# Performance work log

Measured on AMD Instinct MI355X. Metric: run time of the kernel, lower is better.

Reference implementation:

```python
import jax, jax.numpy as jnp
import numpy as np

V, E, U, L = 50000, 512, 20, 9   # vocab, embed dim, user feats, labels
R, S, T = 64, 32, 50             # reviews, sentences/review, tokens/sentence
D = E + U                        # product-encoder input dim


def setup_inputs() -> dict:
    key = jax.random.key(0)
    ks = jax.random.split(key, 16)
    sc = lambda k, shape: (jax.random.normal(k, shape, jnp.float32) * 0.02)
    return {
        "inputs": jax.random.randint(ks[0], (R, S, T), 0, V),
        "user_feats": jax.random.normal(ks[1], (R, U), jnp.float32),
        "embedding": sc(ks[2], (V, E)),
        "w_sent": sc(ks[3], (E, E)), "b_sent": jnp.zeros((E,), jnp.float32),
        "w_rev": sc(ks[4], (E, E)),  "b_rev": jnp.zeros((E,), jnp.float32),
        "w_prod": sc(ks[5], (D, D)), "b_prod": jnp.zeros((D,), jnp.float32),
        "w_rff": sc(ks[6], (D, 1)),  "b_rff": jnp.zeros((1,), jnp.float32),
        "w_pff": sc(ks[7], (D, L)),  "b_pff": jnp.zeros((L,), jnp.float32),
        "user_w": jnp.ones((U,), jnp.float32),
    }


def _masked_mean(x, mask):
    # x: [..., N, F], mask: [..., N] -> [..., F]
    denom = jnp.maximum(mask.sum(-1, keepdims=True), 1.0)
    return (x * mask[..., None]).sum(-2) / denom


def reference(inputs, user_feats, embedding, w_sent, b_sent, w_rev, b_rev,
              w_prod, b_prod, w_rff, b_rff, w_pff, b_pff, user_w):
    dt = embedding.dtype
    tok_mask = (inputs != 0).astype(dt)                      # [R,S,T]
    emb = embedding[inputs]                                  # [R,S,T,E]
    # sentence encoder (DAN): masked mean over tokens + Linear + SELU
    sent_h = jax.nn.selu(_masked_mean(emb, tok_mask) @ w_sent + b_sent)   # [R,S,E]
    # review encoder: masked mean over sentences (r_mask = p.sum(-1) != 0)
    sent_mask = (inputs.sum(-1) != 0).astype(dt)             # [R,S]
    rev_h = jax.nn.selu(_masked_mean(sent_h, sent_mask) @ w_rev + b_rev)  # [R,E]
    # append L2-normalized user feats scaled by learned weights
    norm = jnp.sqrt((user_feats * user_feats).sum(-1, keepdims=True))
    uf = user_feats / jnp.maximum(norm, 1e-12) * user_w      # [R,U]
    p_batch = jnp.concatenate([rev_h, uf], axis=-1)          # [R,D]
    # per-review star head
    r_stars = jax.nn.selu(p_batch @ w_rff + b_rff).squeeze(-1)            # [R]
    # product encoder: plain mean over reviews (no mask) + Linear + SELU
    h_n = jax.nn.selu(p_batch.mean(-2) @ w_prod + b_prod)    # [D]
    p_stars = jax.nn.selu(h_n @ w_pff + b_pff)               # [L]
    return p_stars, r_stars
```

## Files before the change

kernel.cpp:

```cpp
#include <hip/hip_runtime.h>
#include <hip/hip_bf16.h>

#define R_ 64
#define S_ 32
#define T_ 50
#define E_ 512
#define U_ 20
#define D_ 532
#define L_ 9
#define NSENT (R_ * S_)

#define PCHUNK 128
#define NCG 5
#define NKG 5

typedef __attribute__((ext_vector_type(8))) short bf16x8;
typedef __attribute__((ext_vector_type(4))) float f32x4;

__device__ __forceinline__ float selu_f(float x) {
    const float scale = 1.0507009873554805f;
    const float alpha = 1.6732632423543772f;
    return x > 0.0f ? scale * x : scale * alpha * expm1f(x);
}

__global__ __launch_bounds__(256) void k_fused_A(
        const int* __restrict__ inputs,
        const float* __restrict__ emb,
        const float* __restrict__ w_sent,
        const float* __restrict__ w_rev,
        __hip_bfloat16* __restrict__ sent_bf,
        __hip_bfloat16* __restrict__ wT,
        float* __restrict__ smask,
        int* __restrict__ dcount)
{
    const int tid = threadIdx.x;

    if (blockIdx.x >= NSENT) {
        __shared__ float tile[32][33];
        const int b = blockIdx.x - NSENT;
        const int z = b >> 8;
        const float* w = z ? w_rev : w_sent;
        __hip_bfloat16* o = wT + (size_t)z * E_ * E_;
        const int bb = b & 255;
        const int tx = tid & 31, ty = tid >> 5;
        const int k0 = (bb >> 4) * 32, n0 = (bb & 15) * 32;
        #pragma unroll
        for (int i = 0; i < 4; ++i)
            tile[ty + 8 * i][tx] = w[(size_t)(k0 + ty + 8 * i) * E_ + n0 + tx];
        __syncthreads();
        #pragma unroll
        for (int i = 0; i < 4; ++i)
            o[(size_t)(n0 + ty + 8 * i) * E_ + k0 + tx] = __float2bfloat16(tile[tx][ty + 8 * i]);
        return;
    }

    if (blockIdx.x == 0 && tid == 0) *dcount = 0;

    const int sid = blockIdx.x;
    const int base = sid * T_;
    float2 acc = {0.f, 0.f};
    int cnt = 0;
    for (int t = 0; t < T_; ++t) {
        const int tok = inputs[base + t];
        const float m = (tok != 0) ? 1.0f : 0.0f;
        cnt += (tok != 0);
        const float2 v = ((const float2*)(emb + (size_t)tok * E_))[tid];
        acc.x = fmaf(v.x, m, acc.x);
        acc.y = fmaf(v.y, m, acc.y);
    }
    const float inv = 1.0f / fmaxf((float)cnt, 1.0f);
    __hip_bfloat162 h2;
    h2.x = __float2bfloat16(acc.x * inv);
    h2.y = __float2bfloat16(acc.y * inv);
    ((__hip_bfloat162*)(sent_bf + (size_t)sid * E_))[tid] = h2;
    if (tid == 0) smask[sid] = (cnt > 0) ? 1.0f : 0.0f;
}

__global__ __launch_bounds__(256) void k_gemm_sent_mean(
        const __hip_bfloat16* __restrict__ A,
        const __hip_bfloat16* __restrict__ Bt,
        const float* __restrict__ bias,
        const float* __restrict__ smask,
        __hip_bfloat16* __restrict__ mrev)
{
    __shared__ short As[64][40];
    __shared__ short Bs[64][40];
    const int tid  = threadIdx.x;
    const int wid  = tid >> 6;
    const int lane = tid & 63;
    const int wm = wid >> 1, wn = wid & 1;
    const int bm = blockIdx.y * 64, bn = blockIdx.x * 64;

    const int srow = tid >> 2;
    const int soff = (tid & 3) * 8;

    const short* Ag  = (const short*)A;
    const short* Btg = (const short*)Bt;

    f32x4 acc[2][2];
    #pragma unroll
    for (int i = 0; i < 2; ++i)
        #pragma unroll
        for (int j = 0; j < 2; ++j) acc[i][j] = (f32x4){0.f, 0.f, 0.f, 0.f};

    const int fr = lane & 15;
    const int kg = (lane >> 4) * 8;

    for (int k0 = 0; k0 < E_; k0 += 32) {
        __syncthreads();
        *(bf16x8*)&As[srow][soff] = *(const bf16x8*)&Ag[(size_t)(bm + srow) * E_ + k0 + soff];
        *(bf16x8*)&Bs[srow][soff] = *(const bf16x8*)&Btg[(size_t)(bn + srow) * E_ + k0 + soff];
        __syncthreads();
        bf16x8 af0 = *(const bf16x8*)&As[wm * 32 + fr][kg];
        bf16x8 af1 = *(const bf16x8*)&As[wm * 32 + 16 + fr][kg];
        bf16x8 bf0 = *(const bf16x8*)&Bs[wn * 32 + fr][kg];
        bf16x8 bf1 = *(const bf16x8*)&Bs[wn * 32 + 16 + fr][kg];
        acc[0][0] = __builtin_amdgcn_mfma_f32_16x16x32_bf16(af0, bf0, acc[0][0], 0, 0, 0);
        acc[0][1] = __builtin_amdgcn_mfma_f32_16x16x32_bf16(af0, bf1, acc[0][1], 0, 0, 0);
        acc[1][0] = __builtin_amdgcn_mfma_f32_16x16x32_bf16(af1, bf0, acc[1][0], 0, 0, 0);
        acc[1][1] = __builtin_amdgcn_mfma_f32_16x16x32_bf16(af1, bf1, acc[1][1], 0, 0, 0);
    }

    const int rq = (lane >> 4) * 4;
    float m[2][4];
    float msum = 0.f;
    #pragma unroll
    for (int fm = 0; fm < 2; ++fm)
        #pragma unroll
        for (int j = 0; j < 4; ++j) {
            m[fm][j] = smask[bm + wm * 32 + fm * 16 + rq + j];
            msum += m[fm][j];
        }
    float colsum[2];
    #pragma unroll
    for (int fn = 0; fn < 2; ++fn) {
        const float bv = bias[bn + wn * 32 + fn * 16 + fr];
        float s = 0.f;
        #pragma unroll
        for (int fm = 0; fm < 2; ++fm)
            #pragma unroll
            for (int j = 0; j < 4; ++j)
                s = fmaf(selu_f(acc[fm][fn][j] + bv), m[fm][j], s);
        colsum[fn] = s;
    }
    #pragma unroll
    for (int fn = 0; fn < 2; ++fn) {
        colsum[fn] += __shfl_xor(colsum[fn], 16, 64);
        colsum[fn] += __shfl_xor(colsum[fn], 32, 64);
    }
    msum += __shfl_xor(msum, 16, 64);
    msum += __shfl_xor(msum, 32, 64);
    const float inv = 1.0f / fmaxf(msum, 1.0f);
    if (lane < 16) {
        const int g = 2 * blockIdx.y + wm;
        #pragma unroll
        for (int fn = 0; fn < 2; ++fn)
            mrev[(size_t)g * E_ + bn + wn * 32 + fn * 16 + fr] =
                __float2bfloat16(colsum[fn] * inv);
    }
}

__global__ __launch_bounds__(256) void k_gemm_rev(
        const __hip_bfloat16* __restrict__ A,
        const __hip_bfloat16* __restrict__ Bt,
        const float* __restrict__ bias,
        const float* __restrict__ user_feats,
        const float* __restrict__ user_w,
        float* __restrict__ p_batch)
{
    __shared__ short As[64][40];
    __shared__ short Bs[64][40];
    const int tid  = threadIdx.x;
    const int wid  = tid >> 6;
    const int lane = tid & 63;
    const int wm = wid >> 1, wn = wid & 1;
    const int bn = blockIdx.x * 64;

    if (blockIdx.x == 0 && tid < 64) {
        const int r = tid;
        float ss = 0.f;
        #pragma unroll
        for (int j = 0; j < U_; ++j) {
            const float u = user_feats[r * U_ + j];
            ss = fmaf(u, u, ss);
        }
        const float nrm = fmaxf(sqrtf(ss), 1e-12f);
        #pragma unroll
        for (int j = 0; j < U_; ++j)
            p_batch[(size_t)r * D_ + E_ + j] = user_feats[r * U_ + j] / nrm * user_w[j];
    }

    const int srow = tid >> 2;
    const int soff = (tid & 3) * 8;
    const short* Ag  = (const short*)A;
    const short* Btg = (const short*)Bt;

    f32x4 acc[2][2];
    #pragma unroll
    for (int i = 0; i < 2; ++i)
        #pragma unroll
        for (int j = 0; j < 2; ++j) acc[i][j] = (f32x4){0.f, 0.f, 0.f, 0.f};

    const int fr = lane & 15;
    const int kg = (lane >> 4) * 8;

    for (int k0 = 0; k0 < E_; k0 += 32) {
        __syncthreads();
        *(bf16x8*)&As[srow][soff] = *(const bf16x8*)&Ag[(size_t)srow * E_ + k0 + soff];
        *(bf16x8*)&Bs[srow][soff] = *(const bf16x8*)&Btg[(size_t)(bn + srow) * E_ + k0 + soff];
        __syncthreads();
        bf16x8 af0 = *(const bf16x8*)&As[wm * 32 + fr][kg];
        bf16x8 af1 = *(const bf16x8*)&As[wm * 32 + 16 + fr][kg];
        bf16x8 bf0 = *(const bf16x8*)&Bs[wn * 32 + fr][kg];
        bf16x8 bf1 = *(const bf16x8*)&Bs[wn * 32 + 16 + fr][kg];
        acc[0][0] = __builtin_amdgcn_mfma_f32_16x16x32_bf16(af0, bf0, acc[0][0], 0, 0, 0);
        acc[0][1] = __builtin_amdgcn_mfma_f32_16x16x32_bf16(af0, bf1, acc[0][1], 0, 0, 0);
        acc[1][0] = __builtin_amdgcn_mfma_f32_16x16x32_bf16(af1, bf0, acc[1][0], 0, 0, 0);
        acc[1][1] = __builtin_amdgcn_mfma_f32_16x16x32_bf16(af1, bf1, acc[1][1], 0, 0, 0);
    }

    const int rq = (lane >> 4) * 4;
    #pragma unroll
    for (int fm = 0; fm < 2; ++fm) {
        #pragma unroll
        for (int fn = 0; fn < 2; ++fn) {
            const int col = bn + wn * 32 + fn * 16 + fr;
            const float bv = bias[col];
            #pragma unroll
            for (int j = 0; j < 4; ++j) {
                const int row = wm * 32 + fm * 16 + rq + j;
                p_batch[(size_t)row * D_ + col] = selu_f(acc[fm][fn][j] + bv);
            }
        }
    }
}

__global__ __launch_bounds__(256) void k_prod_fused(
        const float* __restrict__ p_batch,
        const float* __restrict__ w_prod,
        const float* __restrict__ b_prod,
        const float* __restrict__ w_pff,
        const float* __restrict__ b_pff,
        const float* __restrict__ w_rff,
        const float* __restrict__ b_rff,
        float* __restrict__ part,
        int* __restrict__ dcount,
        float* __restrict__ out_p,
        float* __restrict__ out_r)
{
    __shared__ float pbar[PCHUNK];
    __shared__ float red[2][PCHUNK];
    const int cg = blockIdx.x, kg = blockIdx.y;
    const int tid = threadIdx.x;
    const int cl = tid & (PCHUNK - 1);
    const int h  = tid >> 7;
    const int k0 = kg * PCHUNK;
    const int klen = min(PCHUNK, D_ - k0);

    if (cl < klen) {
        float s = 0.f;
        #pragma unroll 8
        for (int r = h * 32; r < h * 32 + 32; ++r)
            s += p_batch[(size_t)r * D_ + k0 + cl];
        red[h][cl] = s;
    }
    __syncthreads();
    if (h == 0 && cl < klen) pbar[cl] = (red[0][cl] + red[1][cl]) * (1.0f / 64.0f);
    __syncthreads();

    const int c = cg * PCHUNK + cl;
    float acc = 0.f;
    if (c < D_) {
        const int jb = h * 64;
        const int je = min(jb + 64, klen);
        for (int j = jb; j < je; ++j)
            acc = fmaf(pbar[j], w_prod[(size_t)(k0 + j) * D_ + c], acc);
    }
    red[h][cl] = acc;
    __syncthreads();
    if (h == 0 && c < D_) part[kg * D_ + c] = red[0][cl] + red[1][cl];

    __threadfence();
    __shared__ int is_last;
    if (tid == 0) is_last = (atomicAdd(dcount, 1) == NCG * NKG - 1);
    __syncthreads();
    if (!is_last) return;
    __threadfence();

    __shared__ float hn[D_];
    __shared__ float rred[4][64];
    for (int cc = tid; cc < D_; cc += 256) {
        float s = b_prod[cc];
        #pragma unroll
        for (int g = 0; g < NKG; ++g) s += part[g * D_ + cc];
        hn[cc] = selu_f(s);
    }
    __syncthreads();
    if (tid < L_) {
        float a = 0.f;
        for (int k = 0; k < D_; ++k) a = fmaf(hn[k], w_pff[k * L_ + tid], a);
        out_p[tid] = selu_f(a + b_pff[tid]);
    }
    {
        const int r = tid & 63, q = tid >> 6;
        float pr = 0.f;
        for (int k = q * 133; k < (q + 1) * 133; ++k)
            pr = fmaf(p_batch[(size_t)r * D_ + k], w_rff[k], pr);
        rred[q][r] = pr;
    }
    __syncthreads();
    if (tid < 64)
        out_r[tid] = selu_f(rred[0][tid] + rred[1][tid] + rred[2][tid] + rred[3][tid]
                            + b_rff[0]);
}

extern "C" void kernel_launch(void* const* d_in, const int* in_sizes, int n_in,
                              void* d_out, int out_size, void* d_ws, size_t ws_size,
                              hipStream_t stream) {
    const int*   inputs     = (const int*)  d_in[0];
    const float* user_feats = (const float*)d_in[1];
    const float* emb        = (const float*)d_in[2];
    const float* w_sent     = (const float*)d_in[3];
    const float* b_sent     = (const float*)d_in[4];
    const float* w_rev      = (const float*)d_in[5];
    const float* b_rev      = (const float*)d_in[6];
    const float* w_prod     = (const float*)d_in[7];
    const float* b_prod     = (const float*)d_in[8];
    const float* w_rff      = (const float*)d_in[9];
    const float* b_rff      = (const float*)d_in[10];
    const float* w_pff      = (const float*)d_in[11];
    const float* b_pff      = (const float*)d_in[12];
    const float* user_w     = (const float*)d_in[13];
    float* out = (float*)d_out;

    float* ws = (float*)d_ws;
    __hip_bfloat16* sent_bf = (__hip_bfloat16*)(ws);
    __hip_bfloat16* wT      = (__hip_bfloat16*)(ws + 524288);
    __hip_bfloat16* mrev    = (__hip_bfloat16*)(ws + 786432);
    float* smask   = ws + 802816;
    float* p_batch = ws + 804864;
    float* part    = ws + 838912;
    int*   dcount  = (int*)(ws + 841600);

    k_fused_A<<<NSENT + 512, 256, 0, stream>>>(inputs, emb, w_sent, w_rev,
                                               sent_bf, wT, smask, dcount);
    k_gemm_sent_mean<<<dim3(E_ / 64, NSENT / 64), 256, 0, stream>>>(
        sent_bf, wT, b_sent, smask, mrev);
    k_gemm_rev<<<dim3(E_ / 64, 1), 256, 0, stream>>>(
        mrev, wT + (size_t)E_ * E_, b_rev, user_feats, user_w, p_batch);
    k_prod_fused<<<dim3(NCG, NKG), 256, 0, stream>>>(
        p_batch, w_prod, b_prod, w_pff, b_pff, w_rff, b_rff,
        part, dcount, out, out + L_);
}
```

Before: 81.31 us.

## Fuse review-mean into rev GEMM epilogue and parallelize pff head

The review GEMM now computes the column means of p_batch (including the normalized user features) in its epilogue and writes them to a workspace vector. The product kernel loads that vector instead of re-reading and reducing p_batch in every block. The rev GEMM also uses a 64-wide K step, which halves its barrier count, and the final 9-output pff projection is split over 252 threads with a shared-memory reduction instead of running serially on 9 threads. This trims redundant work and serial tails in small latency-bound kernels, at the cost of extra shared memory and one more barrier in the GEMM.

```diff
diff --git a/kernel.cpp b/kernel.cpp
--- a/kernel.cpp
+++ b/kernel.cpp
@@ -90,21 +90,19 @@
     const int lane = tid & 63;
     const int wm = wid >> 1, wn = wid & 1;
     const int bm = blockIdx.y * 64, bn = blockIdx.x * 64;
-
     const int srow = tid >> 2;
     const int soff = (tid & 3) * 8;
-
     const short* Ag  = (const short*)A;
     const short* Btg = (const short*)Bt;
-
-    f32x4 acc[2][2];
-    #pragma unroll
-    for (int i = 0; i < 2; ++i)
-        #pragma unroll
-        for (int j = 0; j < 2; ++j) acc[i][j] = (f32x4){0.f, 0.f, 0.f, 0.f};
-
     const int fr = lane & 15;
     const int kg = (lane >> 4) * 8;
+    const int rq = (lane >> 4) * 4;
+
+    f32x4 acc[2][2];
+    #pragma unroll
+    for (int i = 0; i < 2; ++i)
+        #pragma unroll
+        for (int j = 0; j < 2; ++j) acc[i][j] = (f32x4){0.f, 0.f, 0.f, 0.f};
 
     for (int k0 = 0; k0 < E_; k0 += 32) {
         __syncthreads();
@@ -121,7 +119,6 @@
         acc[1][1] = __builtin_amdgcn_mfma_f32_16x16x32_bf16(af1, bf1, acc[1][1], 0, 0, 0);
     }
 
-    const int rq = (lane >> 4) * 4;
     float m[2][4];
     float msum = 0.f;
     #pragma unroll
@@ -166,15 +163,23 @@
         const float* __restrict__ bias,
         const float* __restrict__ user_feats,
         const float* __restrict__ user_w,
-        float* __restrict__ p_batch)
+        float* __restrict__ p_batch,
+        float* __restrict__ pbar)
 {
-    __shared__ short As[64][40];
-    __shared__ short Bs[64][40];
+    __shared__ short As[64][72];
+    __shared__ short Bs[64][72];
+    __shared__ float cs[2][2][2][16];
+    __shared__ float ufl[64][U_];
     const int tid  = threadIdx.x;
     const int wid  = tid >> 6;
     const int lane = tid & 63;
     const int wm = wid >> 1, wn = wid & 1;
     const int bn = blockIdx.x * 64;
+    const int fr = lane & 15;
+    const int kg = (lane >> 4) * 8;
+    const int rq = (lane >> 4) * 4;
+    const int srow = tid >> 2;
+    const int scol = (tid & 3) * 8;
 
     if (blockIdx.x == 0 && tid < 64) {
         const int r = tid;
@@ -186,12 +191,13 @@
         }
         const float nrm = fmaxf(sqrtf(ss), 1e-12f);
         #pragma unroll
-        for (int j = 0; j < U_; ++j)
-            p_batch[(size_t)r * D_ + E_ + j] = user_feats[r * U_ + j] / nrm * user_w[j];
-    }
-
-    const int srow = tid >> 2;
-    const int soff = (tid & 3) * 8;
+        for (int j = 0; j < U_; ++j) {
+            const float v = user_feats[r * U_ + j] / nrm * user_w[j];
+            p_batch[(size_t)r * D_ + E_ + j] = v;
+            ufl[r][j] = v;
+        }
+    }
+
     const short* Ag  = (const short*)A;
     const short* Btg = (const short*)Bt;
 
@@ -201,25 +207,27 @@
         #pragma unroll
         for (int j = 0; j < 2; ++j) acc[i][j] = (f32x4){0.f, 0.f, 0.f, 0.f};
 
-    const int fr = lane & 15;
-    const int kg = (lane >> 4) * 8;
-
-    for (int k0 = 0; k0 < E_; k0 += 32) {
-        __syncthreads();
-        *(bf16x8*)&As[srow][soff] = *(const bf16x8*)&Ag[(size_t)srow * E_ + k0 + soff];
-        *(bf16x8*)&Bs[srow][soff] = *(const bf16x8*)&Btg[(size_t)(bn + srow) * E_ + k0 + soff];
-        __syncthreads();
-        bf16x8 af0 = *(const bf16x8*)&As[wm * 32 + fr][kg];
-        bf16x8 af1 = *(const bf16x8*)&As[wm * 32 + 16 + fr][kg];
-        bf16x8 bf0 = *(const bf16x8*)&Bs[wn * 32 + fr][kg];
-        bf16x8 bf1 = *(const bf16x8*)&Bs[wn * 32 + 16 + fr][kg];
-        acc[0][0] = __builtin_amdgcn_mfma_f32_16x16x32_bf16(af0, bf0, acc[0][0], 0, 0, 0);
-        acc[0][1] = __builtin_amdgcn_mfma_f32_16x16x32_bf16(af0, bf1, acc[0][1], 0, 0, 0);
-        acc[1][0] = __builtin_amdgcn_mfma_f32_16x16x32_bf16(af1, bf0, acc[1][0], 0, 0, 0);
-        acc[1][1] = __builtin_amdgcn_mfma_f32_16x16x32_bf16(af1, bf1, acc[1][1], 0, 0, 0);
-    }
-
-    const int rq = (lane >> 4) * 4;
+    for (int k0 = 0; k0 < E_; k0 += 64) {
+        __syncthreads();
+        *(bf16x8*)&As[srow][scol]      = *(const bf16x8*)&Ag[(size_t)srow * E_ + k0 + scol];
+        *(bf16x8*)&As[srow][scol + 32] = *(const bf16x8*)&Ag[(size_t)srow * E_ + k0 + scol + 32];
+        *(bf16x8*)&Bs[srow][scol]      = *(const bf16x8*)&Btg[(size_t)(bn + srow) * E_ + k0 + scol];
+        *(bf16x8*)&Bs[srow][scol + 32] = *(const bf16x8*)&Btg[(size_t)(bn + srow) * E_ + k0 + scol + 32];
+        __syncthreads();
+        #pragma unroll
+        for (int ks = 0; ks < 64; ks += 32) {
+            bf16x8 af0 = *(const bf16x8*)&As[wm * 32 + fr][ks + kg];
+            bf16x8 af1 = *(const bf16x8*)&As[wm * 32 + 16 + fr][ks + kg];
+            bf16x8 bf0 = *(const bf16x8*)&Bs[wn * 32 + fr][ks + kg];
+            bf16x8 bf1 = *(const bf16x8*)&Bs[wn * 32 + 16 + fr][ks + kg];
+            acc[0][0] = __builtin_amdgcn_mfma_f32_16x16x32_bf16(af0, bf0, acc[0][0], 0, 0, 0);
+            acc[0][1] = __builtin_amdgcn_mfma_f32_16x16x32_bf16(af0, bf1, acc[0][1], 0, 0, 0);
+            acc[1][0] = __builtin_amdgcn_mfma_f32_16x16x32_bf16(af1, bf0, acc[1][0], 0, 0, 0);
+            acc[1][1] = __builtin_amdgcn_mfma_f32_16x16x32_bf16(af1, bf1, acc[1][1], 0, 0, 0);
+        }
+    }
+
+    float colsum[2] = {0.f, 0.f};
     #pragma unroll
     for (int fm = 0; fm < 2; ++fm) {
         #pragma unroll
@@ -229,13 +237,37 @@
             #pragma unroll
             for (int j = 0; j < 4; ++j) {
                 const int row = wm * 32 + fm * 16 + rq + j;
-                p_batch[(size_t)row * D_ + col] = selu_f(acc[fm][fn][j] + bv);
+                const float val = selu_f(acc[fm][fn][j] + bv);
+                p_batch[(size_t)row * D_ + col] = val;
+                colsum[fn] += val;
             }
         }
     }
+    #pragma unroll
+    for (int fn = 0; fn < 2; ++fn) {
+        colsum[fn] += __shfl_xor(colsum[fn], 16, 64);
+        colsum[fn] += __shfl_xor(colsum[fn], 32, 64);
+    }
+    if (lane < 16) {
+        cs[wm][wn][0][fr] = colsum[0];
+        cs[wm][wn][1][fr] = colsum[1];
+    }
+    __syncthreads();
+    if (tid < 64) {
+        const int wn2 = tid >> 5, fn2 = (tid >> 4) & 1, fr2 = tid & 15;
+        const float s = cs[0][wn2][fn2][fr2] + cs[1][wn2][fn2][fr2];
+        pbar[bn + wn2 * 32 + fn2 * 16 + fr2] = s * (1.0f / 64.0f);
+    }
+    if (blockIdx.x == 0 && tid < U_) {
+        float s = 0.f;
+        #pragma unroll 16
+        for (int r = 0; r < 64; ++r) s += ufl[r][tid];
+        pbar[E_ + tid] = s * (1.0f / 64.0f);
+    }
 }
 
 __global__ __launch_bounds__(256) void k_prod_fused(
+        const float* __restrict__ pbar_g,
         const float* __restrict__ p_batch,
         const float* __restrict__ w_prod,
         const float* __restrict__ b_prod,
@@ -248,7 +280,7 @@
         float* __restrict__ out_p,
         float* __restrict__ out_r)
 {
-    __shared__ float pbar[PCHUNK];
+    __shared__ float pb[PCHUNK];
     __shared__ float red[2][PCHUNK];
     const int cg = blockIdx.x, kg = blockIdx.y;
     const int tid = threadIdx.x;
@@ -257,15 +289,7 @@
     const int k0 = kg * PCHUNK;
     const int klen = min(PCHUNK, D_ - k0);
 
-    if (cl < klen) {
-        float s = 0.f;
-        #pragma unroll 8
-        for (int r = h * 32; r < h * 32 + 32; ++r)
-            s += p_batch[(size_t)r * D_ + k0 + cl];
-        red[h][cl] = s;
-    }
-    __syncthreads();
-    if (h == 0 && cl < klen) pbar[cl] = (red[0][cl] + red[1][cl]) * (1.0f / 64.0f);
+    if (tid < klen) pb[tid] = pbar_g[k0 + tid];
     __syncthreads();
 
     const int c = cg * PCHUNK + cl;
@@ -274,7 +298,7 @@
         const int jb = h * 64;
         const int je = min(jb + 64, klen);
         for (int j = jb; j < je; ++j)
-            acc = fmaf(pbar[j], w_prod[(size_t)(k0 + j) * D_ + c], acc);
+            acc = fmaf(pb[j], w_prod[(size_t)(k0 + j) * D_ + c], acc);
     }
     red[h][cl] = acc;
     __syncthreads();
@@ -289,6 +313,7 @@
 
     __shared__ float hn[D_];
     __shared__ float rred[4][64];
+    __shared__ float ppart[L_][28];
     for (int cc = tid; cc < D_; cc += 256) {
         float s = b_prod[cc];
         #pragma unroll
@@ -296,10 +321,12 @@
         hn[cc] = selu_f(s);
     }
     __syncthreads();
-    if (tid < L_) {
-        float a = 0.f;
-        for (int k = 0; k < D_; ++k) a = fmaf(hn[k], w_pff[k * L_ + tid], a);
-        out_p[tid] = selu_f(a + b_pff[tid]);
+    if (tid < L_ * 28) {
+        const int o = tid / 28, ii = tid % 28;
+        float s = 0.f;
+        for (int k = ii; k < D_; k += 28)
+            s = fmaf(hn[k], w_pff[(size_t)k * L_ + o], s);
+        ppart[o][ii] = s;
     }
     {
         const int r = tid & 63, q = tid >> 6;
@@ -309,6 +336,12 @@
         rred[q][r] = pr;
     }
     __syncthreads();
+    if (tid < L_) {
+        float s = 0.f;
+        #pragma unroll
+        for (int ii = 0; ii < 28; ++ii) s += ppart[tid][ii];
+        out_p[tid] = selu_f(s + b_pff[tid]);
+    }
     if (tid < 64)
         out_r[tid] = selu_f(rred[0][tid] + rred[1][tid] + rred[2][tid] + rred[3][tid]
                             + b_rff[0]);
@@ -340,15 +373,16 @@
     float* smask   = ws + 802816;
     float* p_batch = ws + 804864;
     float* part    = ws + 838912;
-    int*   dcount  = (int*)(ws + 841600);
+    float* pbar_ws = ws + 841600;
+    int*   dcount  = (int*)(ws + 842144);
 
     k_fused_A<<<NSENT + 512, 256, 0, stream>>>(inputs, emb, w_sent, w_rev,
                                                sent_bf, wT, smask, dcount);
     k_gemm_sent_mean<<<dim3(E_ / 64, NSENT / 64), 256, 0, stream>>>(
         sent_bf, wT, b_sent, smask, mrev);
-    k_gemm_rev<<<dim3(E_ / 64, 1), 256, 0, stream>>>(
-        mrev, wT + (size_t)E_ * E_, b_rev, user_feats, user_w, p_batch);
+    k_gemm_rev<<<dim3(8, 1), 256, 0, stream>>>(
+        mrev, wT + (size_t)E_ * E_, b_rev, user_feats, user_w, p_batch, pbar_ws);
     k_prod_fused<<<dim3(NCG, NKG), 256, 0, stream>>>(
-        p_batch, w_prod, b_prod, w_pff, b_pff, w_rff, b_rff,
+        pbar_ws, p_batch, w_prod, b_prod, w_pff, b_pff, w_rff, b_rff,
         part, dcount, out, out + L_);
 }
```

Measured after the change: 88.60 us. 9.0% more time.
